# Kernel tuning notes

Measured on AMD Instinct MI355X. Metric: run time of the kernel, lower is better.

## Reference

```python
import jax, jax.numpy as jnp
import numpy as np

NU, NS, NT = 200000, 100000, 100000
N = NS + NU + NT          # node order: [source items | users | target items]
D = 32                    # embedding_size
K = 3                     # graph_layer_K
DK = D * (K + 1)          # 128, concat of all propagation layers
META = 64                 # meta_dim
B = 2048                  # batch
L = 50                    # padded history length
NNZ = 2000000             # nnz of normalized adjacency


def setup_inputs() -> dict:
    key = jax.random.key(0)
    ks = jax.random.split(key, 32)
    f = lambda i, shape, s=0.05: jax.random.normal(ks[i], shape, jnp.float32) * s
    z = lambda shape: jnp.zeros(shape, jnp.float32)
    return dict(
        u=jax.random.randint(ks[0], (B,), 0, NU, jnp.int32),
        si=jax.random.randint(ks[1], (B,), 0, NS, jnp.int32),
        ti=jax.random.randint(ks[2], (B,), 0, NT, jnp.int32),
        src_seq=jax.random.randint(ks[3], (NU, L), 0, NS, jnp.int32),
        tgt_seq=jax.random.randint(ks[4], (NU, L), 0, NT, jnp.int32),
        adj_rows=jax.random.randint(ks[5], (NNZ,), 0, N, jnp.int32),
        adj_cols=jax.random.randint(ks[6], (NNZ,), 0, N, jnp.int32),
        adj_vals=jax.random.uniform(ks[7], (NNZ,), jnp.float32) * 0.1,
        user_emb=f(8, (NU, D), 0.1),
        item_s_emb=f(9, (NS, D), 0.1),
        item_t_emb=f(10, (NT, D), 0.1),
        attn_s_w1=f(11, (D, D)), attn_s_b1=z((D,)), attn_s_w2=f(12, (D, 1)),
        attn_t_w1=f(13, (D, D)), attn_t_b1=z((D,)), attn_t_w2=f(14, (D, 1)),
        dec_ss_w1=f(15, (D, META)), dec_ss_b1=z((META,)),
        dec_ss_w2=f(16, (META, DK * DK), 0.02), dec_ss_b2=z((DK * DK,)),
        dec_tt_w1=f(17, (D, META)), dec_tt_b1=z((META,)),
        dec_tt_w2=f(18, (META, DK * DK), 0.02), dec_tt_b2=z((DK * DK,)),
        mlp_s_w1=f(19, (2 * DK, 128)), mlp_s_b1=z((128,)),
        mlp_s_w2=f(20, (128, 64)), mlp_s_b2=z((64,)),
        dense_s_w=f(21, (64, 1)), dense_s_b=z((1,)),
        mlp_t_w1=f(22, (2 * DK, 128)), mlp_t_b1=z((128,)),
        mlp_t_w2=f(23, (128, 64)), mlp_t_b2=z((64,)),
        dense_t_w=f(24, (64, 1)), dense_t_b=z((1,)),
    )


def _attn_pool(seq_ids, item_emb, w1, b1, w2):
    # masked attention pooling over padded history; pad id is 0
    e = item_emb[seq_ids]                          # [B,L,D]
    h = jax.nn.relu(e @ w1 + b1)                   # attention_layer_K = 1
    logits = h @ w2                                # [B,L,1], no bias on final layer
    mask = (seq_ids == 0)[..., None].astype(e.dtype)
    att = jax.nn.softmax(logits - mask * 1e8, axis=1)
    return jnp.sum(att * e, axis=1)                # [B,D]


def _meta_decode(his, w1, b1, w2, b2, u_e):
    # meta-generated per-sample DKxDK transform applied to the user embedding
    W = (jax.nn.relu(his @ w1 + b1) @ w2 + b2).reshape(-1, DK, DK)
    return jnp.einsum('bd,bde->be', u_e, W)


def _ncf(x, w1, b1, w2, b2, dw, db):
    h = jax.nn.relu(x @ w1 + b1)
    h = jax.nn.relu(h @ w2 + b2)
    return jax.nn.sigmoid(h @ dw + db)[:, 0]


def reference(u, si, ti, src_seq, tgt_seq, adj_rows, adj_cols, adj_vals,
              user_emb, item_s_emb, item_t_emb,
              attn_s_w1, attn_s_b1, attn_s_w2, attn_t_w1, attn_t_b1, attn_t_w2,
              dec_ss_w1, dec_ss_b1, dec_ss_w2, dec_ss_b2,
              dec_tt_w1, dec_tt_b1, dec_tt_w2, dec_tt_b2,
              mlp_s_w1, mlp_s_b1, mlp_s_w2, mlp_s_b2, dense_s_w, dense_s_b,
              mlp_t_w1, mlp_t_b1, mlp_t_w2, mlp_t_b2, dense_t_w, dense_t_b):
    his_s = _attn_pool(src_seq[u], item_s_emb, attn_s_w1, attn_s_b1, attn_s_w2)
    his_t = _attn_pool(tgt_seq[u], item_t_emb, attn_t_w1, attn_t_b1, attn_t_w2)

    # 'raw' graph encoder: K hops of sparse A @ E over [item_s | user | item_t]
    emb = jnp.concatenate([item_s_emb, user_emb, item_t_emb], axis=0)  # [N,D]
    all_emb = [emb]
    for _ in range(K):
        emb = jax.ops.segment_sum(adj_vals[:, None] * emb[adj_cols], adj_rows,
                                  num_segments=N)
        all_emb.append(emb)
    all_e = jnp.concatenate(all_emb, axis=1)       # [N, DK]

    si_e = all_e[si]                               # source items: rows [0, NS)
    u_e = all_e[NS + u]                            # users: rows [NS, NS+NU)
    ti_e = all_e[NS + NU + ti]                     # target items

    u_ss = _meta_decode(his_s, dec_ss_w1, dec_ss_b1, dec_ss_w2, dec_ss_b2, u_e)
    u_tt = _meta_decode(his_t, dec_tt_w1, dec_tt_b1, dec_tt_w2, dec_tt_b2, u_e)

    pred_s = _ncf(jnp.concatenate([u_ss, si_e], -1),
                  mlp_s_w1, mlp_s_b1, mlp_s_w2, mlp_s_b2, dense_s_w, dense_s_b)
    pred_t = _ncf(jnp.concatenate([u_tt, ti_e], -1),
                  mlp_t_w1, mlp_t_b1, mlp_t_w2, mlp_t_b2, dense_t_w, dense_t_b)
    return jnp.stack([pred_s, pred_t])             # [2, B]
```

## Files before the change

kernel.cpp:

```cpp
#include <hip/hip_runtime.h>
#include <hip/hip_bf16.h>

#define NU_ 200000
#define NS_ 100000
#define NT_ 100000
#define NN_ (NS_ + NU_ + NT_)
#define D_ 32
#define DK_ 128
#define META_ 64
#define B_ 2048
#define L_ 50
#define NNZ_ 2000000
#define GK_ 8192

#define RPB_ 391
#define NB_ 1024
#define STAGE_CAP_ 4096
#define CAPA_ 1280
#define CAPB_ 512

#define SB_EMB_   6250
#define IN4_SLOT3_ 100096
#define IN4_MARKS_ 50048
#define IN4_E3C_   49152
#define IN4_TOT_  (IN4_SLOT3_ + IN4_MARKS_ + IN4_E3C_)
#define SB_INIT_  ((IN4_TOT_ + 2048 + 255) / 256)
#define SB_TOT_   (SB_EMB_ + SB_INIT_)

#define PB_GATHER_ 192
#define PB_HRELU_  (PB_GATHER_ + 1024)
#define PB_TOT_    (PB_HRELU_ + 1024)

typedef __attribute__((ext_vector_type(8))) short bf16x8;
typedef __attribute__((ext_vector_type(4))) float f32x4;

__device__ inline unsigned bfpack(float a, float b) {
    unsigned ua = __float_as_uint(a), ub = __float_as_uint(b);
    ua += 0x7fffu + ((ua >> 16) & 1u);
    ub += 0x7fffu + ((ub >> 16) & 1u);
    return (ua >> 16) | (ub & 0xffff0000u);
}
__device__ inline float bf2f(short s) {
    return __uint_as_float(((unsigned)(unsigned short)s) << 16);
}

__global__ __launch_bounds__(256) void setup_kernel(
    const float* __restrict__ item_s, const float* __restrict__ user_e,
    const float* __restrict__ item_t, unsigned short* __restrict__ tab,
    int* __restrict__ slot3, int* __restrict__ marks ,
    float* __restrict__ E3c, int* __restrict__ bcurA, int* __restrict__ bcurB)
{
    int bid = blockIdx.x, t = threadIdx.x;
    if (bid < SB_EMB_) {
        int tid = bid * 256 + t;
        int row = tid >> 2, seg = tid & 3;
        const float* src;
        if (row < NS_)            src = item_s + (size_t)row * 32;
        else if (row < NS_ + NU_) src = user_e + (size_t)(row - NS_) * 32;
        else                      src = item_t + (size_t)(row - NS_ - NU_) * 32;
        const float4* sp = (const float4*)(src + seg * 8);
        float4 a = sp[0], b = sp[1];
        uint4 r;
        r.x = bfpack(a.x, a.y); r.y = bfpack(a.z, a.w);
        r.z = bfpack(b.x, b.y); r.w = bfpack(b.z, b.w);
        *(uint4*)(tab + (size_t)row * 32 + seg * 8) = r;
    } else {
        int idx = (bid - SB_EMB_) * 256 + t;
        if (idx < IN4_SLOT3_) {
            ((int4*)slot3)[idx] = make_int4(-1, -1, -1, -1);
        } else if (idx < IN4_SLOT3_ + IN4_MARKS_) {
            ((int4*)marks)[idx - IN4_SLOT3_] = make_int4(0, 0, 0, 0);
        } else if (idx < IN4_TOT_) {
            ((int4*)E3c)[idx - IN4_SLOT3_ - IN4_MARKS_] = make_int4(0, 0, 0, 0);
        } else {
            int c = idx - IN4_TOT_;
            if (c < NB_)            bcurA[c] = c * CAPA_;
            else if (c < 2 * NB_)   bcurB[c - NB_] = (c - NB_) * CAPB_;
        }
    }
}

__global__ __launch_bounds__(256) void mark_seeds(
    const int* __restrict__ u, const int* __restrict__ si, const int* __restrict__ ti,
    int* __restrict__ slot3, unsigned char* __restrict__ mark1,
    unsigned char* __restrict__ mark2)
{
    int n = blockIdx.x * 256 + threadIdx.x;
    if (n >= 3 * B_) return;
    int which = n >> 11, b = n & (B_ - 1);
    int row = (which == 0) ? si[b] : (which == 1) ? NS_ + u[b] : NS_ + NU_ + ti[b];
    slot3[row] = n;
    mark1[row] = 1;
    mark2[row] = 1;
}

__global__ __launch_bounds__(256) void mark_pass(
    const int* __restrict__ rows, const int* __restrict__ cols,
    const int* __restrict__ slot3, const unsigned char* __restrict__ msrc,
    unsigned char* __restrict__ mdst, int use_slot)
{
    int j = blockIdx.x * 256 + threadIdx.x;
    if (j >= NNZ_) return;
    int r = rows[j];
    bool cond = use_slot ? (slot3[r] >= 0) : (msrc[r] != 0);
    if (cond) mdst[cols[j]] = 1;
}

__global__ __launch_bounds__(512) void partition_edges(
    const int* __restrict__ rows, const int* __restrict__ cols,
    const float* __restrict__ vals,
    const unsigned char* __restrict__ mark1, const unsigned char* __restrict__ mark2,
    int* __restrict__ bcurA, int* __restrict__ bcurB,
    int2* __restrict__ partA, int2* __restrict__ partB)
{
    __shared__ int hist[NB_], sstart[NB_], sbase[NB_], scur[NB_];
    __shared__ int2 stage[STAGE_CAP_];
    __shared__ unsigned short stageb[STAGE_CAP_];
    __shared__ int stotal;

    int t = threadIdx.x;
    for (int i = t; i < NB_; i += 512) hist[i] = 0;
    __syncthreads();

    int base = blockIdx.x * 8192;
    int mybkt[16]; int2 mye[16]; unsigned myB = 0;
    #pragma unroll
    for (int i = 0; i < 16; i++) {
        int j = base + i * 512 + t;
        mybkt[i] = -1;
        if (j < NNZ_) {
            int r = rows[j];
            if (mark1[r]) {
                int bb = r / RPB_;
                int lr = r - bb * RPB_;
                mye[i] = make_int2((lr << 19) | cols[j], __float_as_int(vals[j]));
                mybkt[i] = bb;
                if (mark2[r]) myB |= (1u << i);
                atomicAdd(&hist[bb], 1);
            }
        }
    }
    __syncthreads();
    for (int i = t; i < NB_; i += 512) sstart[i] = hist[i];
    __syncthreads();
    for (int off = 1; off < NB_; off <<= 1) {
        int x0 = (t >= off) ? sstart[t - off] : 0;
        int x1 = (t + 512 >= off) ? sstart[t + 512 - off] : 0;
        __syncthreads();
        sstart[t] += x0; sstart[t + 512] += x1;
        __syncthreads();
    }
    if (t == 0) stotal = sstart[NB_ - 1];
    __syncthreads();
    int tot = stotal;
    for (int i = t; i < NB_; i += 512) {
        int cnt = hist[i];
        sstart[i] -= cnt;
        sbase[i] = cnt ? atomicAdd(&bcurA[i], cnt) : 0;
        scur[i] = 0;
    }
    __syncthreads();

    if (tot <= STAGE_CAP_) {
        #pragma unroll
        for (int i = 0; i < 16; i++) {
            int bb = mybkt[i];
            if (bb >= 0) {
                int p = atomicAdd(&scur[bb], 1);
                int s = sstart[bb] + p;
                stage[s] = mye[i];
                stageb[s] = (unsigned short)bb;
            }
        }
        __syncthreads();
        for (int i = t; i < tot; i += 512) {
            int bb = stageb[i];
            int pos = sbase[bb] + (i - sstart[bb]);
            if (pos < (bb + 1) * CAPA_) partA[pos] = stage[i];
        }
    } else {
        #pragma unroll
        for (int i = 0; i < 16; i++) {
            int bb = mybkt[i];
            if (bb >= 0) {
                int p = atomicAdd(&scur[bb], 1);
                int pos = sbase[bb] + p;
                if (pos < (bb + 1) * CAPA_) partA[pos] = mye[i];
            }
        }
    }
    __syncthreads();
    for (int i = t; i < NB_; i += 512) hist[i] = 0;
    __syncthreads();
    #pragma unroll
    for (int i = 0; i < 16; i++)
        if (myB & (1u << i)) atomicAdd(&hist[mybkt[i]], 1);
    __syncthreads();
    for (int i = t; i < NB_; i += 512) {
        sbase[i] = hist[i] ? atomicAdd(&bcurB[i], hist[i]) : 0;
        scur[i] = 0;
    }
    __syncthreads();
    #pragma unroll
    for (int i = 0; i < 16; i++) {
        if (myB & (1u << i)) {
            int bb = mybkt[i];
            int p = atomicAdd(&scur[bb], 1);
            int pos = sbase[bb] + p;
            if (pos < (bb + 1) * CAPB_) partB[pos] = mye[i];
        }
    }
}

__global__ __launch_bounds__(512) void hop_csr(
    const int* __restrict__ bcur, const int2* __restrict__ part, int cap,
    const unsigned short* __restrict__ tab,
    const unsigned char* __restrict__ markw,
    float* __restrict__ yf, unsigned short* __restrict__ ybf)
{
    __shared__ int2 sorted[CAPA_];
    __shared__ int cnt[RPB_];
    __shared__ int scanb[512];

    int t = threadIdx.x;
    int bkt = blockIdx.x;
    int e0 = bkt * cap;
    int n = bcur[bkt] - e0;
    if (n > cap) n = cap;

    for (int i = t; i < RPB_; i += 512) cnt[i] = 0;
    __syncthreads();
    for (int i = t; i < n; i += 512) {
        int lr = (part[e0 + i].x >> 19) & 0x3FF;
        atomicAdd(&cnt[lr], 1);
    }
    __syncthreads();
    scanb[t] = (t < RPB_) ? cnt[t] : 0;
    __syncthreads();
    for (int off = 1; off < 512; off <<= 1) {
        int x = (t >= off) ? scanb[t - off] : 0;
        __syncthreads();
        scanb[t] += x;
        __syncthreads();
    }
    if (t < RPB_) cnt[t] = scanb[t] - cnt[t];
    __syncthreads();
    for (int i = t; i < n; i += 512) {
        int2 e = part[e0 + i];
        int lr = (e.x >> 19) & 0x3FF;
        int p2 = atomicAdd(&cnt[lr], 1);
        sorted[p2] = e;
    }
    __syncthreads();
    int chunk = t & 3;
    int row0 = bkt * RPB_;
    for (int r = t >> 2; r < RPB_; r += 128) {
        int grow = row0 + r;
        if (grow >= NN_ || !markw[grow]) continue;
        int eb = (r == 0) ? 0 : scanb[r - 1];
        int ee = scanb[r];
        float racc[8] = {0.f, 0.f, 0.f, 0.f, 0.f, 0.f, 0.f, 0.f};
        for (int e = eb; e < ee; e++) {
            int2 ed = sorted[e];
            int col = ed.x & 0x7FFFF;
            float vv = __int_as_float(ed.y);
            bf16x8 x = *(const bf16x8*)(tab + (size_t)col * 32 + chunk * 8);
            #pragma unroll
            for (int k = 0; k < 8; k++) racc[k] += vv * bf2f(x[k]);
        }
        float4 o0 = {racc[0], racc[1], racc[2], racc[3]};
        float4 o1 = {racc[4], racc[5], racc[6], racc[7]};
        float4* yp = (float4*)(yf + (size_t)grow * 32 + chunk * 8);
        yp[0] = o0; yp[1] = o1;
        if (ybf) {
            uint4 pk;
            pk.x = bfpack(o0.x, o0.y); pk.y = bfpack(o0.z, o0.w);
            pk.z = bfpack(o1.x, o1.y); pk.w = bfpack(o1.z, o1.w);
            *(uint4*)(ybf + (size_t)grow * 32 + chunk * 8) = pk;
        }
    }
}

__global__ __launch_bounds__(256) void hop3_part(
    const int* __restrict__ bcurB, const int2* __restrict__ partB,
    const int* __restrict__ slot3,
    const float* __restrict__ E2, float* __restrict__ E3c)
{
    int t = threadIdx.x;
    int bkt = blockIdx.x;
    int e0 = bkt * CAPB_;
    int e1 = bcurB[bkt];
    int emax = e0 + CAPB_;
    if (e1 > emax) e1 = emax;
    int c = t & 7;
    for (int i = e0 + (t >> 3); i < e1; i += 32) {
        int2 e = partB[i];
        int lr = (e.x >> 19) & 0x3FF;
        int s = slot3[bkt * RPB_ + lr];
        if (s < 0) continue;
        int col = e.x & 0x7FFFF;
        float v = __int_as_float(e.y);
        float4 xv = ((const float4*)E2)[(size_t)col * 8 + c];
        float* p = E3c + (size_t)s * 32 + c * 4;
        unsafeAtomicAdd(p + 0, v * xv.x);
        unsafeAtomicAdd(p + 1, v * xv.y);
        unsafeAtomicAdd(p + 2, v * xv.z);
        unsafeAtomicAdd(p + 3, v * xv.w);
    }
}

__global__ __launch_bounds__(64) void attn_pool(
    const int* __restrict__ u,
    const int* __restrict__ seq_s, const int* __restrict__ seq_t,
    const float* __restrict__ emb_s, const float* __restrict__ emb_t,
    const float* __restrict__ w1_s, const float* __restrict__ b1_s,
    const float* __restrict__ w2_s,
    const float* __restrict__ w1_t, const float* __restrict__ b1_t,
    const float* __restrict__ w2_t,
    float* __restrict__ out_s, float* __restrict__ out_t)
{
    int b = blockIdx.x, dom = blockIdx.y;
    const int* seq = dom ? seq_t : seq_s;
    const float* emb = dom ? emb_t : emb_s;
    const float* w1 = dom ? w1_t : w1_s;
    const float* b1 = dom ? b1_t : b1_s;
    const float* w2 = dom ? w2_t : w2_s;
    float* out = dom ? out_t : out_s;

    int l = threadIdx.x;
    __shared__ float w1s[32 * 32];
    __shared__ float b1s[32];
    __shared__ float w2s[32];
    __shared__ float es[L_ * 32];
    __shared__ float att[64];

    for (int i = l; i < 1024; i += 64) w1s[i] = w1[i];
    if (l < 32) { b1s[l] = b1[l]; w2s[l] = w2[l]; }
    __syncthreads();

    int uid = u[b];
    float logit = -1e30f;
    if (l < L_) {
        int id = seq[uid * L_ + l];
        const float4* ep = (const float4*)(emb + (size_t)id * 32);
        float e[32];
        #pragma unroll
        for (int q = 0; q < 8; q++) {
            float4 v = ep[q];
            e[4*q+0] = v.x; e[4*q+1] = v.y; e[4*q+2] = v.z; e[4*q+3] = v.w;
        }
        float acc = 0.f;
        #pragma unroll
        for (int i = 0; i < 32; i++) {
            float h = b1s[i];
            #pragma unroll
            for (int jj = 0; jj < 32; jj++) h += e[jj] * w1s[jj * 32 + i];
            h = fmaxf(h, 0.f);
            acc += h * w2s[i];
        }
        logit = acc - (id == 0 ? 1e8f : 0.f);
        #pragma unroll
        for (int jj = 0; jj < 32; jj++) es[l * 32 + jj] = e[jj];
    }
    float m = logit;
    for (int off = 32; off > 0; off >>= 1) m = fmaxf(m, __shfl_down(m, off, 64));
    m = __shfl(m, 0, 64);
    float ex = (l < L_) ? expf(logit - m) : 0.f;
    float s = ex;
    for (int off = 32; off > 0; off >>= 1) s += __shfl_down(s, off, 64);
    s = __shfl(s, 0, 64);
    att[l] = ex / s;
    __syncthreads();

    if (l < 32) {
        float o = 0.f;
        for (int q = 0; q < L_; q++) o += att[q] * es[q * 32 + l];
        out[b * 32 + l] = o;
    }
}

__global__ __launch_bounds__(256) void prep_kernel(
    const float* __restrict__ E1, const float* __restrict__ E2,
    const float* __restrict__ E3c, const int* __restrict__ slot3,
    const int* __restrict__ u, const int* __restrict__ si, const int* __restrict__ ti,
    const float* __restrict__ user_emb, const float* __restrict__ item_s,
    const float* __restrict__ item_t,
    float* __restrict__ u_e, float* __restrict__ si_e, float* __restrict__ ti_e,
    const float* __restrict__ his_s, const float* __restrict__ his_t,
    const float* __restrict__ dw1_s, const float* __restrict__ db1_s,
    const float* __restrict__ dw1_t, const float* __restrict__ db1_t,
    float* __restrict__ h_s, float* __restrict__ h_t,
    const float* __restrict__ w2_s, const float* __restrict__ w2_t,
    unsigned short* __restrict__ o_s, unsigned short* __restrict__ o_t)
{
    int bid = blockIdx.x, t = threadIdx.x;
    if (bid < PB_GATHER_) {
        int tid = bid * 256 + t;
        if (tid >= 3 * B_ * 8) return;
        int n = tid >> 3, c = tid & 7;
        int which = n >> 11, b = n & (B_ - 1);
        int row;
        const float4* base0;
        float* outp;
        if (which == 0)      { int id = si[b]; row = id;             base0 = (const float4*)item_s + (size_t)id * 8; outp = si_e; }
        else if (which == 1) { int id = u[b];  row = NS_ + id;       base0 = (const float4*)user_emb + (size_t)id * 8; outp = u_e; }
        else                 { int id = ti[b]; row = NS_ + NU_ + id; base0 = (const float4*)item_t + (size_t)id * 8; outp = ti_e; }
        float4 k0 = base0[c];
        float4 k1 = ((const float4*)E1)[(size_t)row * 8 + c];
        float4 k2 = ((const float4*)E2)[(size_t)row * 8 + c];
        float4 k3 = ((const float4*)E3c)[(size_t)slot3[row] * 8 + c];
        float4* orow = (float4*)(outp + (size_t)b * 128);
        orow[0 * 8 + c] = k0;
        orow[1 * 8 + c] = k1;
        orow[2 * 8 + c] = k2;
        orow[3 * 8 + c] = k3;
    } else if (bid < PB_HRELU_) {
        int b2 = bid - PB_GATHER_;
        int dom = b2 >> 9, sub = b2 & 511;
        const float* his = dom ? his_t : his_s;
        const float* w1  = dom ? dw1_t : dw1_s;
        const float* b1  = dom ? db1_t : db1_s;
        float* h         = dom ? h_t   : h_s;
        int b = sub * 4 + (t >> 6);
        int m = t & 63;
        float acc = b1[m];
        #pragma unroll
        for (int j = 0; j < 32; j++) acc += his[b * 32 + j] * w1[j * 64 + m];
        h[b * 64 + m] = fmaxf(acc, 0.f);
    } else {
        int b3 = bid - PB_HRELU_;
        int dom = b3 >> 9, sub = b3 & 511;
        const float* w2 = dom ? w2_t : w2_s;
        unsigned short* o = dom ? o_t : o_s;
        int tid = sub * 256 + t;
        int nn = tid & 127, k8 = tid >> 7;
        float v[8];
        #pragma unroll
        for (int i = 0; i < 8; i++) v[i] = w2[(size_t)(k8 * 8 + i) * 128 + nn];
        uint4 r;
        r.x = bfpack(v[0], v[1]); r.y = bfpack(v[2], v[3]);
        r.z = bfpack(v[4], v[5]); r.w = bfpack(v[6], v[7]);
        *(uint4*)(o + (size_t)nn * GK_ + k8 * 8) = r;
    }
}

__global__ __launch_bounds__(256) void meta_gemm(
    const float* __restrict__ h_s, const float* __restrict__ h_t,
    const float* __restrict__ ue,
    const unsigned short* __restrict__ w2t_s, const unsigned short* __restrict__ w2t_t,
    float* __restrict__ P)
{
    __shared__ unsigned short As[64 * 72];
    __shared__ unsigned short Bs[128 * 72];

    int mt = blockIdx.x & 31, dom = blockIdx.x >> 5;
    int ks = blockIdx.y;
    const float* h = dom ? h_t : h_s;
    const unsigned short* w2t = dom ? w2t_t : w2t_s;

    int t = threadIdx.x;
    int ar = t >> 2, aseg = t & 3;
    int bn = t >> 1, bhalf = t & 1;
    int w = t >> 6, lane = t & 63;
    int quad = lane >> 4, l16 = lane & 15;
    int wm = (w & 1) * 32, wn = (w >> 1) * 64;

    f32x4 acc[8];
    #pragma unroll
    for (int i = 0; i < 8; i++) { acc[i][0]=0.f; acc[i][1]=0.f; acc[i][2]=0.f; acc[i][3]=0.f; }

    for (int ch = 0; ch < 16; ch++) {
        int kb = ks * 1024 + ch * 64;
        __syncthreads();
        {
            int gm = mt * 64 + ar;
            int m_idx = kb >> 7;
            int d0 = (kb & 127) + aseg * 16;
            float hv = h[gm * 64 + m_idx];
            const float4* up = (const float4*)(ue + (size_t)gm * 128 + d0);
            float4 x0 = up[0], x1 = up[1], x2 = up[2], x3 = up[3];
            uint4 A0, A1;
            A0.x = bfpack(hv*x0.x, hv*x0.y); A0.y = bfpack(hv*x0.z, hv*x0.w);
            A0.z = bfpack(hv*x1.x, hv*x1.y); A0.w = bfpack(hv*x1.z, hv*x1.w);
            A1.x = bfpack(hv*x2.x, hv*x2.y); A1.y = bfpack(hv*x2.z, hv*x2.w);
            A1.z = bfpack(hv*x3.x, hv*x3.y); A1.w = bfpack(hv*x3.z, hv*x3.w);
            uint4* sa = (uint4*)(As + ar * 72 + aseg * 16);
            sa[0] = A0; sa[1] = A1;
        }
        {
            const uint4* gb = (const uint4*)(w2t + (size_t)bn * GK_ + kb + bhalf * 32);
            uint4* sb = (uint4*)(Bs + bn * 72 + bhalf * 32);
            sb[0] = gb[0]; sb[1] = gb[1]; sb[2] = gb[2]; sb[3] = gb[3];
        }
        __syncthreads();
        #pragma unroll
        for (int kk = 0; kk < 2; kk++) {
            int ko = kk * 32 + quad * 8;
            bf16x8 a0 = *(const bf16x8*)(As + (wm + l16) * 72 + ko);
            bf16x8 a1 = *(const bf16x8*)(As + (wm + 16 + l16) * 72 + ko);
            #pragma unroll
            for (int nt = 0; nt < 4; nt++) {
                bf16x8 bfr = *(const bf16x8*)(Bs + (wn + nt * 16 + l16) * 72 + ko);
                acc[nt]     = __builtin_amdgcn_mfma_f32_16x16x32_bf16(a0, bfr, acc[nt],     0, 0, 0);
                acc[4 + nt] = __builtin_amdgcn_mfma_f32_16x16x32_bf16(a1, bfr, acc[4 + nt], 0, 0, 0);
            }
        }
    }
    float* op = P + ((size_t)dom * 8 + ks) * B_ * 128;
    #pragma unroll
    for (int ma = 0; ma < 2; ma++)
        #pragma unroll
        for (int nt = 0; nt < 4; nt++) {
            int row = mt * 64 + wm + ma * 16 + quad * 4;
            int col = wn + nt * 16 + l16;
            f32x4 v = acc[ma * 4 + nt];
            op[(size_t)(row + 0) * 128 + col] = v[0];
            op[(size_t)(row + 1) * 128 + col] = v[1];
            op[(size_t)(row + 2) * 128 + col] = v[2];
            op[(size_t)(row + 3) * 128 + col] = v[3];
        }
}

__global__ __launch_bounds__(128) void ncf_kernel(
    const float* __restrict__ P, const float* __restrict__ u_e,
    const float* __restrict__ b2_s, const float* __restrict__ b2_t,
    const float* __restrict__ si_e, const float* __restrict__ ti_e,
    const float* __restrict__ w1_s, const float* __restrict__ b1_s,
    const float* __restrict__ w2_s, const float* __restrict__ bb2_s,
    const float* __restrict__ dw_s, const float* __restrict__ db_s,
    const float* __restrict__ w1_t, const float* __restrict__ b1_t,
    const float* __restrict__ w2_t, const float* __restrict__ bb2_t,
    const float* __restrict__ dw_t, const float* __restrict__ db_t,
    float* __restrict__ out)
{
    int b = blockIdx.x, dom = blockIdx.y, t = threadIdx.x;
    const float* Pd     = P + (size_t)dom * 8 * B_ * 128;
    const float* b2meta = dom ? b2_t : b2_s;
    const float* pair_e = dom ? ti_e : si_e;
    const float* w1 = dom ? w1_t : w1_s;
    const float* b1 = dom ? b1_t : b1_s;
    const float* w2 = dom ? w2_t : w2_s;
    const float* bb2 = dom ? bb2_t : bb2_s;
    const float* dw = dom ? dw_t : dw_s;
    const float* db = dom ? db_t : db_s;

    __shared__ float x[256];
    __shared__ float h1[128];
    __shared__ float h2[64];

    const float* ue = u_e + (size_t)b * 128;
    float bias = 0.f;
    for (int d = 0; d < 128; d++) bias += ue[d] * b2meta[d * 128 + t];
    float s = 0.f;
    #pragma unroll
    for (int ks = 0; ks < 8; ks++) s += Pd[(size_t)ks * B_ * 128 + (size_t)b * 128 + t];
    x[t]       = s + bias;
    x[128 + t] = pair_e[(size_t)b * 128 + t];
    __syncthreads();

    float a1 = b1[t];
    for (int jj = 0; jj < 256; jj++) a1 += x[jj] * w1[jj * 128 + t];
    h1[t] = fmaxf(a1, 0.f);
    __syncthreads();

    if (t < 64) {
        float a2 = bb2[t];
        for (int jj = 0; jj < 128; jj++) a2 += h1[jj] * w2[jj * 64 + t];
        h2[t] = fmaxf(a2, 0.f);
    }
    __syncthreads();

    if (t == 0) {
        float z = db[0];
        for (int jj = 0; jj < 64; jj++) z += h2[jj] * dw[jj];
        out[(size_t)dom * B_ + b] = 1.f / (1.f + expf(-z));
    }
}

extern "C" void kernel_launch(void* const* d_in, const int* in_sizes, int n_in,
                              void* d_out, int out_size, void* d_ws, size_t ws_size,
                              hipStream_t stream)
{
    const int*   u          = (const int*)  d_in[0];
    const int*   si         = (const int*)  d_in[1];
    const int*   ti         = (const int*)  d_in[2];
    const int*   src_seq    = (const int*)  d_in[3];
    const int*   tgt_seq    = (const int*)  d_in[4];
    const int*   adj_rows   = (const int*)  d_in[5];
    const int*   adj_cols   = (const int*)  d_in[6];
    const float* adj_vals   = (const float*)d_in[7];
    const float* user_emb   = (const float*)d_in[8];
    const float* item_s_emb = (const float*)d_in[9];
    const float* item_t_emb = (const float*)d_in[10];
    const float* attn_s_w1  = (const float*)d_in[11];
    const float* attn_s_b1  = (const float*)d_in[12];
    const float* attn_s_w2  = (const float*)d_in[13];
    const float* attn_t_w1  = (const float*)d_in[14];
    const float* attn_t_b1  = (const float*)d_in[15];
    const float* attn_t_w2  = (const float*)d_in[16];
    const float* dec_ss_w1  = (const float*)d_in[17];
    const float* dec_ss_b1  = (const float*)d_in[18];
    const float* dec_ss_w2  = (const float*)d_in[19];
    const float* dec_ss_b2  = (const float*)d_in[20];
    const float* dec_tt_w1  = (const float*)d_in[21];
    const float* dec_tt_b1  = (const float*)d_in[22];
    const float* dec_tt_w2  = (const float*)d_in[23];
    const float* dec_tt_b2  = (const float*)d_in[24];
    const float* mlp_s_w1   = (const float*)d_in[25];
    const float* mlp_s_b1   = (const float*)d_in[26];
    const float* mlp_s_w2   = (const float*)d_in[27];
    const float* mlp_s_b2   = (const float*)d_in[28];
    const float* dense_s_w  = (const float*)d_in[29];
    const float* dense_s_b  = (const float*)d_in[30];
    const float* mlp_t_w1   = (const float*)d_in[31];
    const float* mlp_t_b1   = (const float*)d_in[32];
    const float* mlp_t_w2   = (const float*)d_in[33];
    const float* mlp_t_b2   = (const float*)d_in[34];
    const float* dense_t_w  = (const float*)d_in[35];
    const float* dense_t_b  = (const float*)d_in[36];

    char* p = (char*)d_ws;
    float* E1    = (float*)p;              p += (size_t)NN_ * 32 * 4;
    float* E2    = (float*)p;              p += (size_t)NN_ * 32 * 4;
    unsigned short* Ebf  = (unsigned short*)p; p += (size_t)NN_ * 32 * 2;
    unsigned short* E1bf = (unsigned short*)p; p += (size_t)NN_ * 32 * 2;
    int2*  partA = (int2*)p;               p += (size_t)NB_ * CAPA_ * 8;
    int2*  partB = (int2*)p;               p += (size_t)NB_ * CAPB_ * 8;
    int*   slot3 = (int*)p;                p += (size_t)400384 * 4;
    int*   marks = (int*)p;
    unsigned char* mark1 = (unsigned char*)p; p += 400384;
    unsigned char* mark2 = (unsigned char*)p; p += 400384;
    float* E3c   = (float*)p;              p += (size_t)3 * B_ * 32 * 4;
    int*   bcurA = (int*)p;                p += NB_ * 4;
    int*   bcurB = (int*)p;                p += NB_ * 4;
    float* his_s = (float*)p;              p += (size_t)B_ * 32 * 4;
    float* his_t = (float*)p;              p += (size_t)B_ * 32 * 4;
    float* u_e   = (float*)p;              p += (size_t)B_ * 128 * 4;
    float* si_e  = (float*)p;              p += (size_t)B_ * 128 * 4;
    float* ti_e  = (float*)p;              p += (size_t)B_ * 128 * 4;
    float* h_s   = (float*)p;              p += (size_t)B_ * 64 * 4;
    float* h_t   = (float*)p;              p += (size_t)B_ * 64 * 4;
    float* P     = (float*)p;              p += (size_t)2 * 8 * B_ * 128 * 4;
    unsigned short* w2t_s = (unsigned short*)p; p += (size_t)128 * GK_ * 2;
    unsigned short* w2t_t = (unsigned short*)p; p += (size_t)128 * GK_ * 2;

    int nnzBlocks = (NNZ_ + 255) / 256;

    setup_kernel<<<SB_TOT_, 256, 0, stream>>>(item_s_emb, user_emb, item_t_emb,
                                              Ebf, slot3, marks, E3c, bcurA, bcurB);
    mark_seeds<<<24, 256, 0, stream>>>(u, si, ti, slot3, mark1, mark2);
    mark_pass<<<nnzBlocks, 256, 0, stream>>>(adj_rows, adj_cols, slot3, mark2, mark2, 1);
    mark_pass<<<nnzBlocks, 256, 0, stream>>>(adj_rows, adj_cols, slot3, mark2, mark1, 0);
    partition_edges<<<245, 512, 0, stream>>>(adj_rows, adj_cols, adj_vals,
                                             mark1, mark2, bcurA, bcurB, partA, partB);
    hop_csr<<<NB_, 512, 0, stream>>>(bcurA, partA, CAPA_, Ebf,  mark1, E1, E1bf);
    hop_csr<<<NB_, 512, 0, stream>>>(bcurB, partB, CAPB_, E1bf, mark2, E2, nullptr);
    hop3_part<<<NB_, 256, 0, stream>>>(bcurB, partB, slot3, E2, E3c);
    attn_pool<<<dim3(B_, 2), 64, 0, stream>>>(u, src_seq, tgt_seq,
                                              item_s_emb, item_t_emb,
                                              attn_s_w1, attn_s_b1, attn_s_w2,
                                              attn_t_w1, attn_t_b1, attn_t_w2,
                                              his_s, his_t);
    prep_kernel<<<PB_TOT_, 256, 0, stream>>>(E1, E2, E3c, slot3, u, si, ti,
                                             user_emb, item_s_emb, item_t_emb,
                                             u_e, si_e, ti_e,
                                             his_s, his_t,
                                             dec_ss_w1, dec_ss_b1,
                                             dec_tt_w1, dec_tt_b1, h_s, h_t,
                                             dec_ss_w2, dec_tt_w2, w2t_s, w2t_t);
    meta_gemm<<<dim3(64, 8), 256, 0, stream>>>(h_s, h_t, u_e, w2t_s, w2t_t, P);
    ncf_kernel<<<dim3(B_, 2), 128, 0, stream>>>(P, u_e, dec_ss_b2, dec_tt_b2,
                                                si_e, ti_e,
                                                mlp_s_w1, mlp_s_b1, mlp_s_w2, mlp_s_b2,
                                                dense_s_w, dense_s_b,
                                                mlp_t_w1, mlp_t_b1, mlp_t_w2, mlp_t_b2,
                                                dense_t_w, dense_t_b,
                                                (float*)d_out);
}
```

Measured before the change: 429.9 us.

## Tile NCF kernel over 16 batch rows to reuse weight loads

The NCF head kernel now processes 16 batch rows per 512-thread block instead of one row per 128-thread block. Each weight element of the bias projection and both MLP layers is loaded once and applied to 4 (or 2) rows held in registers, with activations staged in shared memory and read as float4. The final dot product uses a warp shuffle reduction. This cuts redundant global weight traffic per row, at the cost of fewer blocks (256) and more shared memory per block.

```diff
diff --git a/kernel.cpp b/kernel.cpp
--- a/kernel.cpp
+++ b/kernel.cpp
@@ -30,6 +30,8 @@
 #define PB_GATHER_ 192
 #define PB_HRELU_  (PB_GATHER_ + 1024)
 #define PB_TOT_    (PB_HRELU_ + 1024)
+
+#define NCF_TILE_ 16
 
 typedef __attribute__((ext_vector_type(8))) short bf16x8;
 typedef __attribute__((ext_vector_type(4))) float f32x4;
@@ -521,7 +523,7 @@
         }
 }
 
-__global__ __launch_bounds__(128) void ncf_kernel(
+__global__ __launch_bounds__(512) void ncf_kernel(
     const float* __restrict__ P, const float* __restrict__ u_e,
     const float* __restrict__ b2_s, const float* __restrict__ b2_t,
     const float* __restrict__ si_e, const float* __restrict__ ti_e,
@@ -533,7 +535,8 @@
     const float* __restrict__ dw_t, const float* __restrict__ db_t,
     float* __restrict__ out)
 {
-    int b = blockIdx.x, dom = blockIdx.y, t = threadIdx.x;
+    int tile = blockIdx.x, dom = blockIdx.y, t = threadIdx.x;
+    int b0 = tile * NCF_TILE_;
     const float* Pd     = P + (size_t)dom * 8 * B_ * 128;
     const float* b2meta = dom ? b2_t : b2_s;
     const float* pair_e = dom ? ti_e : si_e;
@@ -544,36 +547,98 @@
     const float* dw = dom ? dw_t : dw_s;
     const float* db = dom ? db_t : db_s;
 
-    __shared__ float x[256];
-    __shared__ float h1[128];
-    __shared__ float h2[64];
-
-    const float* ue = u_e + (size_t)b * 128;
-    float bias = 0.f;
-    for (int d = 0; d < 128; d++) bias += ue[d] * b2meta[d * 128 + t];
-    float s = 0.f;
-    #pragma unroll
-    for (int ks = 0; ks < 8; ks++) s += Pd[(size_t)ks * B_ * 128 + (size_t)b * 128 + t];
-    x[t]       = s + bias;
-    x[128 + t] = pair_e[(size_t)b * 128 + t];
-    __syncthreads();
-
-    float a1 = b1[t];
-    for (int jj = 0; jj < 256; jj++) a1 += x[jj] * w1[jj * 128 + t];
-    h1[t] = fmaxf(a1, 0.f);
-    __syncthreads();
-
-    if (t < 64) {
-        float a2 = bb2[t];
-        for (int jj = 0; jj < 128; jj++) a2 += h1[jj] * w2[jj * 64 + t];
-        h2[t] = fmaxf(a2, 0.f);
-    }
-    __syncthreads();
-
-    if (t == 0) {
-        float z = db[0];
-        for (int jj = 0; jj < 64; jj++) z += h2[jj] * dw[jj];
-        out[(size_t)dom * B_ + b] = 1.f / (1.f + expf(-z));
+    __shared__ float ues[NCF_TILE_ * 128];
+    __shared__ float xs[NCF_TILE_ * 256];
+    __shared__ float h1s[NCF_TILE_ * 128];
+    __shared__ float h2s[NCF_TILE_ * 64];
+
+    {
+        float4 v = ((const float4*)(u_e + (size_t)b0 * 128))[t];
+        ((float4*)ues)[t] = v;
+        float4 pv = ((const float4*)(pair_e + (size_t)b0 * 128))[t];
+        int s = t >> 5, c4 = t & 31;
+        ((float4*)(xs + s * 256 + 128))[c4] = pv;
+    }
+    __syncthreads();
+
+    int j = t & 127, g = t >> 7;
+    {
+        float acc[4];
+        #pragma unroll
+        for (int ss = 0; ss < 4; ss++) {
+            int b = b0 + g * 4 + ss;
+            float a = 0.f;
+            #pragma unroll
+            for (int ks = 0; ks < 8; ks++)
+                a += Pd[(size_t)ks * B_ * 128 + (size_t)b * 128 + j];
+            acc[ss] = a;
+        }
+        for (int dc = 0; dc < 32; dc++) {
+            float wa = b2meta[(dc * 4 + 0) * 128 + j];
+            float wb = b2meta[(dc * 4 + 1) * 128 + j];
+            float wc = b2meta[(dc * 4 + 2) * 128 + j];
+            float wd = b2meta[(dc * 4 + 3) * 128 + j];
+            #pragma unroll
+            for (int ss = 0; ss < 4; ss++) {
+                float4 uv = ((const float4*)(ues + (g * 4 + ss) * 128))[dc];
+                acc[ss] += uv.x * wa + uv.y * wb + uv.z * wc + uv.w * wd;
+            }
+        }
+        #pragma unroll
+        for (int ss = 0; ss < 4; ss++) xs[(g * 4 + ss) * 256 + j] = acc[ss];
+    }
+    __syncthreads();
+
+    {
+        float b1v = b1[j];
+        float acc[4] = {b1v, b1v, b1v, b1v};
+        for (int kc = 0; kc < 64; kc++) {
+            float wa = w1[(kc * 4 + 0) * 128 + j];
+            float wb = w1[(kc * 4 + 1) * 128 + j];
+            float wc = w1[(kc * 4 + 2) * 128 + j];
+            float wd = w1[(kc * 4 + 3) * 128 + j];
+            #pragma unroll
+            for (int ss = 0; ss < 4; ss++) {
+                float4 xv = ((const float4*)(xs + (g * 4 + ss) * 256))[kc];
+                acc[ss] += xv.x * wa + xv.y * wb + xv.z * wc + xv.w * wd;
+            }
+        }
+        #pragma unroll
+        for (int ss = 0; ss < 4; ss++)
+            h1s[(g * 4 + ss) * 128 + j] = fmaxf(acc[ss], 0.f);
+    }
+    __syncthreads();
+
+    {
+        int m = t & 63, g2 = t >> 6;
+        float bv = bb2[m];
+        float acc[2] = {bv, bv};
+        for (int kc = 0; kc < 32; kc++) {
+            float wa = w2[(kc * 4 + 0) * 64 + m];
+            float wb = w2[(kc * 4 + 1) * 64 + m];
+            float wc = w2[(kc * 4 + 2) * 64 + m];
+            float wd = w2[(kc * 4 + 3) * 64 + m];
+            #pragma unroll
+            for (int ss = 0; ss < 2; ss++) {
+                float4 hv = ((const float4*)(h1s + (g2 * 2 + ss) * 128))[kc];
+                acc[ss] += hv.x * wa + hv.y * wb + hv.z * wc + hv.w * wd;
+            }
+        }
+        #pragma unroll
+        for (int ss = 0; ss < 2; ss++)
+            h2s[(g2 * 2 + ss) * 64 + m] = fmaxf(acc[ss], 0.f);
+    }
+    __syncthreads();
+
+    {
+        int s = t >> 5, l = t & 31;
+        float sum = h2s[s * 64 + l] * dw[l] + h2s[s * 64 + 32 + l] * dw[32 + l];
+        #pragma unroll
+        for (int off = 16; off > 0; off >>= 1) sum += __shfl_down(sum, off, 32);
+        if (l == 0) {
+            float z = sum + db[0];
+            out[(size_t)dom * B_ + b0 + s] = 1.f / (1.f + expf(-z));
+        }
     }
 }
 
@@ -669,7 +734,7 @@
                                              dec_tt_w1, dec_tt_b1, h_s, h_t,
                                              dec_ss_w2, dec_tt_w2, w2t_s, w2t_t);
     meta_gemm<<<dim3(64, 8), 256, 0, stream>>>(h_s, h_t, u_e, w2t_s, w2t_t, P);
-    ncf_kernel<<<dim3(B_, 2), 128, 0, stream>>>(P, u_e, dec_ss_b2, dec_tt_b2,
+    ncf_kernel<<<dim3(B_ / NCF_TILE_, 2), 512, 0, stream>>>(P, u_e, dec_ss_b2, dec_tt_b2,
                                                 si_e, ti_e,
                                                 mlp_s_w1, mlp_s_b1, mlp_s_w2, mlp_s_b2,
                                                 dense_s_w, dense_s_b,
```

New measurement: 427.2 us. Within noise of the previous version (-0.6%).
